# Kernel tuning notes

Hardware: AMD Instinct MI355X
Metric: run time of the kernel (lower is better)

The kernel has to match this reference:

```python
import jax, jax.numpy as jnp
import numpy as np

N = 50000       # num nodes
E = 800000      # num edges (before self loops)
D_IN = 128
D_H = 128
D_OUT = 40


def setup_inputs() -> dict:
    key = jax.random.key(0)
    ks = jax.random.split(key, 8)
    x = jax.random.normal(ks[0], (N, D_IN), dtype=jnp.float32)
    edge_index = jax.random.randint(ks[1], (2, E), 0, N, dtype=jnp.int32)
    # GCNConv weights (glorot-ish scale) and biases
    W1 = jax.random.normal(ks[2], (D_IN, D_H), dtype=jnp.float32) / np.sqrt(D_IN)
    b1 = jnp.zeros((D_H,), dtype=jnp.float32)
    W2 = jax.random.normal(ks[3], (D_H, D_H), dtype=jnp.float32) / np.sqrt(D_H)
    b2 = jnp.zeros((D_H,), dtype=jnp.float32)
    Wc = jax.random.normal(ks[4], (D_H, D_OUT), dtype=jnp.float32) / np.sqrt(D_H)
    bc = jnp.zeros((D_OUT,), dtype=jnp.float32)
    return {"x": x, "edge_index": edge_index, "W1": W1, "b1": b1,
            "W2": W2, "b2": b2, "Wc": Wc, "bc": bc}


def _gcn_conv(x, row, col, num_nodes, W, b):
    # PyG GCNConv: h = X @ W; out[c] += norm(r,c) * h[r]; out += b
    h = x @ W
    deg = jax.ops.segment_sum(jnp.ones(row.shape[0], h.dtype), col,
                              num_segments=num_nodes)
    dinv = jnp.where(deg > 0, jax.lax.rsqrt(deg), 0.0).astype(h.dtype)
    norm = dinv[row] * dinv[col]                      # [E+N]
    msg = h[row] * norm[:, None]                      # gather + scale
    agg = jax.ops.segment_sum(msg, col, num_segments=num_nodes)  # scatter-add
    return agg + b


def reference(x, edge_index, W1, b1, W2, b2, Wc, bc):
    # add self loops (GCNConv default add_self_loops=True)
    loops = jnp.arange(N, dtype=edge_index.dtype)
    row = jnp.concatenate([edge_index[0], loops])
    col = jnp.concatenate([edge_index[1], loops])
    h = jax.nn.relu(_gcn_conv(x, row, col, N, W1, b1))
    h = jax.nn.relu(_gcn_conv(h, row, col, N, W2, b2))
    g = jnp.mean(h, axis=0)                           # mean pool over nodes
    return g @ Wc + bc                                # [D_OUT]
```

## Files before the change

### kernel.cpp

```cpp
#include <hip/hip_runtime.h>
#include <hip/hip_fp16.h>


typedef _Float16 half8 __attribute__((ext_vector_type(8)));
typedef float f32x4 __attribute__((ext_vector_type(4)));
typedef float f32x2 __attribute__((ext_vector_type(2)));

constexpr int N = 50000;
constexpr int E = 800000;
constexpr int D = 128;
constexpr int DOUT = 40;
constexpr int CAP = 64;
constexpr int HB = 128;
constexpr int EPB = E / HB;
constexpr int HWRD = 12500;
constexpr int GM = (N + 127) / 128;
constexpr int NW = N / 4;
constexpr int T4 = E / 4;
constexpr int GF = 3 * GM;

__global__ __launch_bounds__(1024) void k_hist(const int* __restrict__ col,
                                               unsigned char* __restrict__ hist,
                                               unsigned char* __restrict__ rank,
                                               const float* __restrict__ W1,
                                               const float* __restrict__ W2,
                                               __half* __restrict__ T1,
                                               __half* __restrict__ T2) {
    __shared__ unsigned int h[HWRD];
    int b = blockIdx.x, t = threadIdx.x;
    if (b >= HB) {
        int o = (b - HB) * 1024 + t;
        const float* W = (o < 16384) ? W1 : W2;
        __half* T = (o < 16384) ? T1 : T2;
        int oo = o & 16383;
        int n = oo >> 7, k = oo & 127;
        T[oo] = (__half)W[k * 128 + n];
        return;
    }
    for (int i = t; i < HWRD; i += 1024) h[i] = 0;
    __syncthreads();
    int e0 = b * EPB;
    for (int e = e0 + t; e < e0 + EPB; e += 1024) {
        int c = col[e];
        unsigned int old = atomicAdd(&h[c >> 2], 1u << ((c & 3) * 8));
        rank[e] = (unsigned char)((old >> ((c & 3) * 8)) & 0xff);
    }
    __syncthreads();
    unsigned int* out = (unsigned int*)(hist + (size_t)b * 50000);
    for (int i = t; i < HWRD; i += 1024) out[i] = h[i];
}

__global__ void k_colscan(unsigned char* __restrict__ hist, int* __restrict__ deg,
                          float* __restrict__ dinv) {
    int c = blockIdx.x * 256 + threadIdx.x;
    if (c >= N) return;
    int sum = 0;
#pragma unroll 4
    for (int b = 0; b < HB; ++b) {
        size_t idx = (size_t)b * 50000 + c;
        int v = hist[idx];
        hist[idx] = (unsigned char)sum;
        sum += v;
    }
    deg[c] = sum;
    dinv[c] = rsqrtf((float)(sum + 1));
}

__device__ __forceinline__ unsigned char f8enc(float v) {
    return (unsigned char)(__builtin_amdgcn_cvt_pk_fp8_f32(v, v, 0, false) & 0xff);
}
__device__ __forceinline__ void add8f8(float* a, uint2 u) {
    f32x2 f0 = __builtin_amdgcn_cvt_pk_f32_fp8(u.x, false);
    f32x2 f1 = __builtin_amdgcn_cvt_pk_f32_fp8(u.x, true);
    f32x2 f2 = __builtin_amdgcn_cvt_pk_f32_fp8(u.y, false);
    f32x2 f3 = __builtin_amdgcn_cvt_pk_f32_fp8(u.y, true);
    a[0] += f0[0]; a[1] += f0[1]; a[2] += f1[0]; a[3] += f1[1];
    a[4] += f2[0]; a[5] += f2[1]; a[6] += f3[0]; a[7] += f3[1];
}

__device__ __forceinline__ half8 ldA(const float* rowp, int koff) {
    float4 u0 = *(const float4*)(rowp + koff);
    float4 u1 = *(const float4*)(rowp + koff + 4);
    half8 r;
    r[0] = (_Float16)u0.x; r[1] = (_Float16)u0.y;
    r[2] = (_Float16)u0.z; r[3] = (_Float16)u0.w;
    r[4] = (_Float16)u1.x; r[5] = (_Float16)u1.y;
    r[6] = (_Float16)u1.z; r[7] = (_Float16)u1.w;
    return r;
}
__device__ __forceinline__ half8 ldA(const __half* rowp, int koff) {
    return *(const half8*)(rowp + koff);
}

template <typename TA>
__device__ __forceinline__ void mfma_gemm(const TA* __restrict__ A,
                                          const __half* __restrict__ Wt,
                                          const float* __restrict__ dinv,
                                          unsigned char* __restrict__ out8,
                                          int row0, int tid) {
    int wave = tid >> 6, lane = tid & 63;
    int quad = lane >> 4, c16 = lane & 15;
    int m0 = row0 + wave * 32;
    int ra = m0 + c16;      if (ra >= N) ra = 0;
    int rb = m0 + 16 + c16; if (rb >= N) rb = 0;
    const TA* pa = A + (size_t)ra * D;
    const TA* pb = A + (size_t)rb * D;

    f32x4 acc[2][8];
#pragma unroll
    for (int i = 0; i < 2; ++i)
#pragma unroll
        for (int j = 0; j < 8; ++j) acc[i][j] = (f32x4){0.f, 0.f, 0.f, 0.f};

#pragma unroll
    for (int kq = 0; kq < 4; ++kq) {
        int koff = kq * 32 + quad * 8;
        half8 a0 = ldA(pa, koff);
        half8 a1 = ldA(pb, koff);
#pragma unroll
        for (int nt = 0; nt < 8; ++nt) {
            half8 bf = *(const half8*)(Wt + (size_t)(nt * 16 + c16) * D + koff);
            acc[0][nt] = __builtin_amdgcn_mfma_f32_16x16x32_f16(a0, bf, acc[0][nt], 0, 0, 0);
            acc[1][nt] = __builtin_amdgcn_mfma_f32_16x16x32_f16(a1, bf, acc[1][nt], 0, 0, 0);
        }
    }

#pragma unroll
    for (int rt = 0; rt < 2; ++rt) {
        int mt = m0 + rt * 16;
#pragma unroll
        for (int i = 0; i < 4; ++i) {
            int grow = mt + quad * 4 + i;
            if (grow < N) {
                float s = dinv[grow];
                unsigned char* orow = out8 + (size_t)grow * D + c16;
#pragma unroll
                for (int nt = 0; nt < 8; ++nt)
                    orow[nt * 16] = f8enc(acc[rt][nt][i] * s);
            }
        }
    }
}

__global__ __launch_bounds__(256) void k_fuse(const int* __restrict__ ei,
                                              const unsigned char* __restrict__ hist,
                                              const unsigned char* __restrict__ rank,
                                              unsigned short* __restrict__ csr,
                                              const float* __restrict__ x,
                                              const __half* __restrict__ Wt1,
                                              const float* __restrict__ dinv,
                                              unsigned char* __restrict__ out8) {
    int b = blockIdx.x, m = b % 3;
    if (m < 2) {
        int sb = (b / 3) * 2 + m;
        int t = sb * 256 + threadIdx.x;
        if (t >= T4) return;
#pragma unroll
        for (int i = 0; i < 4; ++i) {
            int e = t + i * T4;
            int c = ei[E + e];
            int r = ei[e];
            int chunk = e / EPB;
            int slot = (int)hist[(size_t)chunk * 50000 + c] + (int)rank[e];
            if (slot < CAP) csr[(c << 6) + slot] = (unsigned short)r;
        }
        return;
    }
    mfma_gemm<float>(x, Wt1, dinv, out8, (b / 3) * 128, threadIdx.x);
}

__global__ __launch_bounds__(256) void k_gemm(const __half* __restrict__ A,
                                              const __half* __restrict__ Wt,
                                              const float* __restrict__ dinv,
                                              unsigned char* __restrict__ out8) {
    mfma_gemm<__half>(A, Wt, dinv, out8, blockIdx.x * 128, threadIdx.x);
}

__device__ __forceinline__ float agg_core(int c, int lane,
                                          const unsigned char* __restrict__ hs8,
                                          const int* __restrict__ deg,
                                          const unsigned short* __restrict__ csr,
                                          float* a0) {
    int qw = lane >> 4;
    int q  = lane & 15;
    int dgRaw = deg[c];
    int dg = dgRaw < CAP ? dgRaw : CAP;
    float dc = rsqrtf((float)(dgRaw + 1));
    int e0 = c << 6;

    float a1[8] = {0, 0, 0, 0, 0, 0, 0, 0};
    float a2[8] = {0, 0, 0, 0, 0, 0, 0, 0};
    float a3[8] = {0, 0, 0, 0, 0, 0, 0, 0};
#pragma unroll
    for (int t = 0; t < 8; ++t) a0[t] = 0.f;
    if (qw == 0)
        add8f8(a0, *(const uint2*)&hs8[(size_t)c * D + q * 8]);

    int j = 0;
    for (; j + 16 <= dg; j += 16) {
        int r0 = csr[e0 + j + qw];
        int r1 = csr[e0 + j + 4 + qw];
        int r2 = csr[e0 + j + 8 + qw];
        int r3 = csr[e0 + j + 12 + qw];
        uint2 u0 = *(const uint2*)&hs8[(size_t)r0 * D + q * 8];
        uint2 u1 = *(const uint2*)&hs8[(size_t)r1 * D + q * 8];
        uint2 u2 = *(const uint2*)&hs8[(size_t)r2 * D + q * 8];
        uint2 u3 = *(const uint2*)&hs8[(size_t)r3 * D + q * 8];
        add8f8(a0, u0); add8f8(a1, u1); add8f8(a2, u2); add8f8(a3, u3);
    }
    if (j + 8 <= dg) {
        int r0 = csr[e0 + j + qw];
        int r1 = csr[e0 + j + 4 + qw];
        uint2 u0 = *(const uint2*)&hs8[(size_t)r0 * D + q * 8];
        uint2 u1 = *(const uint2*)&hs8[(size_t)r1 * D + q * 8];
        add8f8(a0, u0); add8f8(a1, u1);
        j += 8;
    }
    if (j + 4 <= dg) {
        int r0 = csr[e0 + j + qw];
        add8f8(a0, *(const uint2*)&hs8[(size_t)r0 * D + q * 8]);
        j += 4;
    }
    int rem = dg - j;
    if (qw < rem) {
        int r0 = csr[e0 + j + qw];
        add8f8(a1, *(const uint2*)&hs8[(size_t)r0 * D + q * 8]);
    }

#pragma unroll
    for (int t = 0; t < 8; ++t) a0[t] += a1[t];
#pragma unroll
    for (int t = 0; t < 8; ++t) a2[t] += a3[t];
#pragma unroll
    for (int t = 0; t < 8; ++t) a0[t] += a2[t];
#pragma unroll
    for (int t = 0; t < 8; ++t) a0[t] += __shfl_xor(a0[t], 16, 64);
#pragma unroll
    for (int t = 0; t < 8; ++t) a0[t] += __shfl_xor(a0[t], 32, 64);
    return dc;
}

__global__ __launch_bounds__(256) void k_agg1(const unsigned char* __restrict__ hs8,
                                              const int* __restrict__ deg,
                                              const unsigned short* __restrict__ csr,
                                              const float* __restrict__ bias,
                                              __half* __restrict__ outH) {
    int wave = threadIdx.x >> 6;
    int lane = threadIdx.x & 63;
    int c = blockIdx.x * 4 + wave;
    float a0[8];
    float dc = agg_core(c, lane, hs8, deg, csr, a0);
    if ((lane >> 4) == 0) {
        int q = lane & 15;
        union { __half2 h[4]; uint4 u; } p;
#pragma unroll
        for (int i = 0; i < 4; ++i) {
            float xv = fmaxf(fmaf(dc, a0[2 * i],     bias[q * 8 + 2 * i]),     0.f);
            float yv = fmaxf(fmaf(dc, a0[2 * i + 1], bias[q * 8 + 2 * i + 1]), 0.f);
            p.h[i] = __floats2half2_rn(xv, yv);
        }
        *(uint4*)&outH[(size_t)c * D + q * 8] = p.u;
    }
}

__global__ __launch_bounds__(256) void k_agg2(const unsigned char* __restrict__ hs8,
                                              const int* __restrict__ deg,
                                              const unsigned short* __restrict__ csr,
                                              const float* __restrict__ bias,
                                              float* __restrict__ gpart) {
    __shared__ float gblk[4][128];
    int wave = threadIdx.x >> 6;
    int lane = threadIdx.x & 63;
    int c = blockIdx.x * 4 + wave;
    float a0[8];
    float dc = agg_core(c, lane, hs8, deg, csr, a0);
    if ((lane >> 4) == 0) {
        int q = lane & 15;
#pragma unroll
        for (int i = 0; i < 8; ++i)
            gblk[wave][q * 8 + i] = fmaxf(fmaf(dc, a0[i], bias[q * 8 + i]), 0.f);
    }
    __syncthreads();
    int t = threadIdx.x;
    if (t < 128)
        gpart[(size_t)blockIdx.x * 128 + t] =
            gblk[0][t] + gblk[1][t] + gblk[2][t] + gblk[3][t];
}

__global__ __launch_bounds__(256) void k_pool(const float* __restrict__ gpart,
                                              float* __restrict__ gpart2) {
    int d = threadIdx.x & 127;
    int half = threadIdx.x >> 7;
    int b = blockIdx.x;
    int per = (NW + 255) / 256;
    int r0 = b * per;
    int r1 = r0 + per;
    if (r1 > NW) r1 = NW;
    float acc = 0.f;
    for (int r = r0 + half; r < r1; r += 2)
        acc += gpart[(size_t)r * D + d];
    __shared__ float red[256];
    red[threadIdx.x] = acc;
    __syncthreads();
    if (half == 0) gpart2[(size_t)b * D + d] = red[d] + red[128 + d];
}

__global__ __launch_bounds__(512) void k_final(const float* __restrict__ gpart2,
                                               const float* __restrict__ Wc,
                                               const float* __restrict__ bc,
                                               float* __restrict__ out) {
    __shared__ float g[D];
    __shared__ float red[512];
    int t = threadIdx.x;
    int d = t & 127, grp = t >> 7;
    float s = 0.f;
#pragma unroll 4
    for (int w = grp * 64; w < grp * 64 + 64; ++w)
        s += gpart2[(size_t)w * D + d];
    red[t] = s;
    __syncthreads();
    if (grp == 0)
        g[d] = (red[d] + red[128 + d] + red[256 + d] + red[384 + d]) * (1.0f / (float)N);
    __syncthreads();
    if (t < DOUT) {
        float acc = bc[t];
        for (int dd = 0; dd < D; ++dd) acc = fmaf(g[dd], Wc[dd * DOUT + t], acc);
        out[t] = acc;
    }
}

extern "C" void kernel_launch(void* const* d_in, const int* in_sizes, int n_in,
                              void* d_out, int out_size, void* d_ws, size_t ws_size,
                              hipStream_t stream) {
    const float* x  = (const float*)d_in[0];
    const int*   ei = (const int*)d_in[1];
    const float* W1 = (const float*)d_in[2];
    const float* b1 = (const float*)d_in[3];
    const float* W2 = (const float*)d_in[4];
    const float* b2 = (const float*)d_in[5];
    const float* Wc = (const float*)d_in[6];
    const float* bc = (const float*)d_in[7];
    float* out = (float*)d_out;

    char* ws = (char*)d_ws;
    size_t off = 0;
    auto alloc = [&](size_t bytes) {
        void* p = ws + off;
        off += (bytes + 511) & ~(size_t)511;
        return p;
    };
    unsigned char*  hist   = (unsigned char*) alloc((size_t)HB * 50000);
    unsigned char*  rank   = (unsigned char*) alloc((size_t)E);
    int*            deg    = (int*)           alloc((size_t)N * 4);
    float*          dinv   = (float*)         alloc((size_t)N * 4);
    unsigned short* csr    = (unsigned short*)alloc((size_t)N * CAP * 2);
    unsigned char*  hs8    = (unsigned char*) alloc((size_t)N * D);
    __half*         hactH  = (__half*)        alloc((size_t)N * D * 2);
    __half*         Wt1    = (__half*)        alloc((size_t)D * D * 2);
    __half*         Wt2    = (__half*)        alloc((size_t)D * D * 2);
    float*          gpart  = (float*)         alloc((size_t)NW * D * 4);
    float*          gpart2 = (float*)         alloc((size_t)256 * D * 4);
    (void)ws_size; (void)in_sizes; (void)n_in; (void)out_size;

    const int* col = ei + E;

    k_hist<<<HB + 32, 1024, 0, stream>>>(col, hist, rank, W1, W2, Wt1, Wt2);
    k_colscan<<<(N + 255) / 256, 256, 0, stream>>>(hist, deg, dinv);
    k_fuse<<<GF, 256, 0, stream>>>(ei, hist, rank, csr, x, Wt1, dinv, hs8);

    k_agg1<<<NW, 256, 0, stream>>>(hs8, deg, csr, b1, hactH);
    k_gemm<<<GM, 256, 0, stream>>>(hactH, Wt2, dinv, hs8);
    k_agg2<<<NW, 256, 0, stream>>>(hs8, deg, csr, b2, gpart);
    k_pool<<<256, 256, 0, stream>>>(gpart, gpart2);
    k_final<<<1, 512, 0, stream>>>(gpart2, Wc, bc, out);
}
```

Baseline: 210.5 us.

## Fuse layer-1 aggregation with layer-2 GEMM and vectorize colscan and CSR fill

Merges the first aggregation and the second-layer GEMM into one kernel. Each 512-thread block aggregates 32 nodes into a shared-memory fp16 tile, then runs the MFMA multiply by W2 and writes fp8 output directly, so the fp16 intermediate activation never makes a global round trip and one launch disappears. The column scan now handles four packed byte counters per 32-bit word, relying on per-chunk counts staying below 256. The CSR fill loads edges, columns and ranks as contiguous vectors. In exchange, the fused kernel does its aggregation serially, four nodes per wave, with a block barrier before the GEMM, which may lower parallelism compared with the separate kernels.

Measured after the change: 213.6 us. No clear change (+1.5%).

```diff
diff --git a/kernel.cpp b/kernel.cpp
--- a/kernel.cpp
+++ b/kernel.cpp
@@ -16,8 +16,8 @@
 constexpr int HWRD = 12500;
 constexpr int GM = (N + 127) / 128;
 constexpr int NW = N / 4;
-constexpr int T4 = E / 4;
 constexpr int GF = 3 * GM;
+constexpr int GB2 = (N + 31) / 32;
 
 __global__ __launch_bounds__(1024) void k_hist(const int* __restrict__ col,
                                                unsigned char* __restrict__ hist,
@@ -52,18 +52,22 @@
 
 __global__ void k_colscan(unsigned char* __restrict__ hist, int* __restrict__ deg,
                           float* __restrict__ dinv) {
-    int c = blockIdx.x * 256 + threadIdx.x;
-    if (c >= N) return;
-    int sum = 0;
-#pragma unroll 4
+    int c4 = blockIdx.x * 256 + threadIdx.x;
+    if (c4 >= HWRD) return;
+    unsigned int* hw = (unsigned int*)hist;
+    unsigned int run = 0;
+#pragma unroll 8
     for (int b = 0; b < HB; ++b) {
-        size_t idx = (size_t)b * 50000 + c;
-        int v = hist[idx];
-        hist[idx] = (unsigned char)sum;
-        sum += v;
-    }
-    deg[c] = sum;
-    dinv[c] = rsqrtf((float)(sum + 1));
+        unsigned int v = hw[b * HWRD + c4];
+        hw[b * HWRD + c4] = run;
+        run += v;
+    }
+#pragma unroll
+    for (int j = 0; j < 4; ++j) {
+        int dg = (run >> (8 * j)) & 0xff;
+        deg[4 * c4 + j] = dg;
+        dinv[4 * c4 + j] = rsqrtf((float)(dg + 1));
+    }
 }
 
 __device__ __forceinline__ unsigned char f8enc(float v) {
@@ -88,12 +92,8 @@
     r[6] = (_Float16)u1.z; r[7] = (_Float16)u1.w;
     return r;
 }
-__device__ __forceinline__ half8 ldA(const __half* rowp, int koff) {
-    return *(const half8*)(rowp + koff);
-}
-
-template <typename TA>
-__device__ __forceinline__ void mfma_gemm(const TA* __restrict__ A,
+
+__device__ __forceinline__ void mfma_gemm(const float* __restrict__ A,
                                           const __half* __restrict__ Wt,
                                           const float* __restrict__ dinv,
                                           unsigned char* __restrict__ out8,
@@ -103,8 +103,8 @@
     int m0 = row0 + wave * 32;
     int ra = m0 + c16;      if (ra >= N) ra = 0;
     int rb = m0 + 16 + c16; if (rb >= N) rb = 0;
-    const TA* pa = A + (size_t)ra * D;
-    const TA* pb = A + (size_t)rb * D;
+    const float* pa = A + (size_t)ra * D;
+    const float* pb = A + (size_t)rb * D;
 
     f32x4 acc[2][8];
 #pragma unroll
@@ -153,27 +153,25 @@
     int b = blockIdx.x, m = b % 3;
     if (m < 2) {
         int sb = (b / 3) * 2 + m;
-        int t = sb * 256 + threadIdx.x;
-        if (t >= T4) return;
+        int e0 = sb * 1024 + threadIdx.x * 4;
+        if (e0 >= E) return;
+        int4 rr = *(const int4*)(ei + e0);
+        int4 cc = *(const int4*)(ei + E + e0);
+        uchar4 kk = *(const uchar4*)(rank + e0);
+        int rs[4] = {rr.x, rr.y, rr.z, rr.w};
+        int cs[4] = {cc.x, cc.y, cc.z, cc.w};
+        int ks[4] = {kk.x, kk.y, kk.z, kk.w};
 #pragma unroll
         for (int i = 0; i < 4; ++i) {
-            int e = t + i * T4;
-            int c = ei[E + e];
-            int r = ei[e];
+            int e = e0 + i;
+            int c = cs[i];
             int chunk = e / EPB;
-            int slot = (int)hist[(size_t)chunk * 50000 + c] + (int)rank[e];
-            if (slot < CAP) csr[(c << 6) + slot] = (unsigned short)r;
+            int slot = (int)hist[(size_t)chunk * 50000 + c] + ks[i];
+            if (slot < CAP) csr[(c << 6) + slot] = (unsigned short)rs[i];
         }
         return;
     }
-    mfma_gemm<float>(x, Wt1, dinv, out8, (b / 3) * 128, threadIdx.x);
-}
-
-__global__ __launch_bounds__(256) void k_gemm(const __half* __restrict__ A,
-                                              const __half* __restrict__ Wt,
-                                              const float* __restrict__ dinv,
-                                              unsigned char* __restrict__ out8) {
-    mfma_gemm<__half>(A, Wt, dinv, out8, blockIdx.x * 128, threadIdx.x);
+    mfma_gemm(x, Wt1, dinv, out8, (b / 3) * 128, threadIdx.x);
 }
 
 __device__ __forceinline__ float agg_core(int c, int lane,
@@ -240,26 +238,60 @@
     return dc;
 }
 
-__global__ __launch_bounds__(256) void k_agg1(const unsigned char* __restrict__ hs8,
-                                              const int* __restrict__ deg,
-                                              const unsigned short* __restrict__ csr,
-                                              const float* __restrict__ bias,
-                                              __half* __restrict__ outH) {
-    int wave = threadIdx.x >> 6;
-    int lane = threadIdx.x & 63;
-    int c = blockIdx.x * 4 + wave;
-    float a0[8];
-    float dc = agg_core(c, lane, hs8, deg, csr, a0);
-    if ((lane >> 4) == 0) {
-        int q = lane & 15;
-        union { __half2 h[4]; uint4 u; } p;
-#pragma unroll
-        for (int i = 0; i < 4; ++i) {
-            float xv = fmaxf(fmaf(dc, a0[2 * i],     bias[q * 8 + 2 * i]),     0.f);
-            float yv = fmaxf(fmaf(dc, a0[2 * i + 1], bias[q * 8 + 2 * i + 1]), 0.f);
-            p.h[i] = __floats2half2_rn(xv, yv);
+__global__ __launch_bounds__(512) void k_agg1g(const unsigned char* __restrict__ hs8,
+                                               const int* __restrict__ deg,
+                                               const unsigned short* __restrict__ csr,
+                                               const float* __restrict__ bias,
+                                               const __half* __restrict__ Wt2,
+                                               const float* __restrict__ dinv,
+                                               unsigned char* __restrict__ out8) {
+    __shared__ __align__(16) __half As[32][136];
+    int wave = threadIdx.x >> 6, lane = threadIdx.x & 63;
+    int n0 = blockIdx.x * 32;
+    int q = lane & 15;
+#pragma unroll 1
+    for (int i = 0; i < 4; ++i) {
+        int c = n0 + wave * 4 + i;
+        if (c < N) {
+            float a0[8];
+            float dc = agg_core(c, lane, hs8, deg, csr, a0);
+            if ((lane >> 4) == 0) {
+                union { __half2 h[4]; uint4 u; } p;
+#pragma unroll
+                for (int j2 = 0; j2 < 4; ++j2) {
+                    float xv = fmaxf(fmaf(dc, a0[2 * j2],     bias[q * 8 + 2 * j2]),     0.f);
+                    float yv = fmaxf(fmaf(dc, a0[2 * j2 + 1], bias[q * 8 + 2 * j2 + 1]), 0.f);
+                    p.h[j2] = __floats2half2_rn(xv, yv);
+                }
+                *(uint4*)&As[wave * 4 + i][q * 8] = p.u;
+            }
+        } else if ((lane >> 4) == 0) {
+            uint4 z = {0, 0, 0, 0};
+            *(uint4*)&As[wave * 4 + i][q * 8] = z;
         }
-        *(uint4*)&outH[(size_t)c * D + q * 8] = p.u;
+    }
+    __syncthreads();
+    int quad = lane >> 4, c16 = lane & 15;
+    f32x4 acc0 = (f32x4){0.f, 0.f, 0.f, 0.f};
+    f32x4 acc1 = (f32x4){0.f, 0.f, 0.f, 0.f};
+    const __half* bcol = Wt2 + (size_t)(wave * 16 + c16) * D;
+#pragma unroll
+    for (int kq = 0; kq < 4; ++kq) {
+        int koff = kq * 32 + quad * 8;
+        half8 a0 = *(const half8*)&As[c16][koff];
+        half8 a1 = *(const half8*)&As[16 + c16][koff];
+        half8 bf = *(const half8*)(bcol + koff);
+        acc0 = __builtin_amdgcn_mfma_f32_16x16x32_f16(a0, bf, acc0, 0, 0, 0);
+        acc1 = __builtin_amdgcn_mfma_f32_16x16x32_f16(a1, bf, acc1, 0, 0, 0);
+    }
+#pragma unroll
+    for (int i = 0; i < 4; ++i) {
+        int g0 = n0 + quad * 4 + i;
+        if (g0 < N)
+            out8[(size_t)g0 * D + wave * 16 + c16] = f8enc(acc0[i] * dinv[g0]);
+        int g1 = n0 + 16 + quad * 4 + i;
+        if (g1 < N)
+            out8[(size_t)g1 * D + wave * 16 + c16] = f8enc(acc1[i] * dinv[g1]);
     }
 }
 
@@ -355,7 +387,7 @@
     float*          dinv   = (float*)         alloc((size_t)N * 4);
     unsigned short* csr    = (unsigned short*)alloc((size_t)N * CAP * 2);
     unsigned char*  hs8    = (unsigned char*) alloc((size_t)N * D);
-    __half*         hactH  = (__half*)        alloc((size_t)N * D * 2);
+    unsigned char*  hs8b   = (unsigned char*) alloc((size_t)N * D);
     __half*         Wt1    = (__half*)        alloc((size_t)D * D * 2);
     __half*         Wt2    = (__half*)        alloc((size_t)D * D * 2);
     float*          gpart  = (float*)         alloc((size_t)NW * D * 4);
@@ -365,12 +397,10 @@
     const int* col = ei + E;
 
     k_hist<<<HB + 32, 1024, 0, stream>>>(col, hist, rank, W1, W2, Wt1, Wt2);
-    k_colscan<<<(N + 255) / 256, 256, 0, stream>>>(hist, deg, dinv);
+    k_colscan<<<(HWRD + 255) / 256, 256, 0, stream>>>(hist, deg, dinv);
     k_fuse<<<GF, 256, 0, stream>>>(ei, hist, rank, csr, x, Wt1, dinv, hs8);
-
-    k_agg1<<<NW, 256, 0, stream>>>(hs8, deg, csr, b1, hactH);
-    k_gemm<<<GM, 256, 0, stream>>>(hactH, Wt2, dinv, hs8);
-    k_agg2<<<NW, 256, 0, stream>>>(hs8, deg, csr, b2, gpart);
+    k_agg1g<<<GB2, 512, 0, stream>>>(hs8, deg, csr, b1, Wt2, dinv, hs8b);
+    k_agg2<<<NW, 256, 0, stream>>>(hs8b, deg, csr, b2, gpart);
     k_pool<<<256, 256, 0, stream>>>(gpart, gpart2);
     k_final<<<1, 512, 0, stream>>>(gpart2, Wc, bc, out);
 }
```
